# Optimization experiments

Measured on AMD Instinct MI355X. Metric: run time of the kernel, lower is better.

The kernel has to match this reference:

```python
import jax, jax.numpy as jnp
import numpy as np

B, N, M, C = 4, 2048, 576, 512
H, KVH, D = 8, 2, 64          # heads, kv heads, head_dim
E, TOPK, F = 8, 2, 2048       # experts, top-k, expert hidden (4*C)
EPS = 1e-6
NEG = -1e9


def setup_inputs() -> dict:
    key = jax.random.key(0)
    ks = iter(jax.random.split(key, 40))
    w = lambda shape, s=0.02: jax.random.normal(next(ks), shape, jnp.float32) * s
    d = {
        'x': jax.random.normal(next(ks), (B, N, C), jnp.float32),
        'vision_features': jax.random.normal(next(ks), (B, M, C), jnp.float32),
        'ln1_g': jnp.ones((C,), jnp.float32), 'ln1_b': jnp.zeros((C,), jnp.float32),
        'ln2_g': jnp.ones((C,), jnp.float32), 'ln2_b': jnp.zeros((C,), jnp.float32),
        'ln3_g': jnp.ones((C,), jnp.float32), 'ln3_b': jnp.zeros((C,), jnp.float32),
        # self-attention (GQA): q -> C, k/v -> KVH*D
        'sa_wq': w((C, C)), 'sa_bq': jnp.zeros((C,), jnp.float32),
        'sa_wk': w((C, KVH * D)), 'sa_bk': jnp.zeros((KVH * D,), jnp.float32),
        'sa_wv': w((C, KVH * D)), 'sa_bv': jnp.zeros((KVH * D,), jnp.float32),
        'sa_wo': w((C, C)), 'sa_bo': jnp.zeros((C,), jnp.float32),
        # cross-attention (GQA)
        'ca_wq': w((C, C)), 'ca_bq': jnp.zeros((C,), jnp.float32),
        'ca_wk': w((C, KVH * D)), 'ca_bk': jnp.zeros((KVH * D,), jnp.float32),
        'ca_wv': w((C, KVH * D)), 'ca_bv': jnp.zeros((KVH * D,), jnp.float32),
        'ca_wo': w((C, C)), 'ca_bo': jnp.zeros((C,), jnp.float32),
        # MoE: router + stacked expert MLPs (C -> F -> C, GELU)
        'router_w': w((C, E)), 'router_b': jnp.zeros((E,), jnp.float32),
        'e_w1': w((E, C, F)), 'e_b1': jnp.zeros((E, F), jnp.float32),
        'e_w2': w((E, F, C)), 'e_b2': jnp.zeros((E, C), jnp.float32),
    }
    return d


def _ln(x, g, b):
    mu = jnp.mean(x, -1, keepdims=True)
    var = jnp.mean(jnp.square(x - mu), -1, keepdims=True)
    return (x - mu) * jax.lax.rsqrt(var + EPS) * g + b


def _gqa_attn(xq, ctx, wq, bq, wk, bk, wv, bv, wo, bo, causal):
    b, n, c = xq.shape
    m = ctx.shape[1]
    q = (xq @ wq + bq).reshape(b, n, H, D).transpose(0, 2, 1, 3)      # bhnd
    k = (ctx @ wk + bk).reshape(b, m, KVH, D).transpose(0, 2, 1, 3)   # bgmd
    v = (ctx @ wv + bv).reshape(b, m, KVH, D).transpose(0, 2, 1, 3)
    rep = H // KVH
    k = jnp.repeat(k, rep, axis=1)  # repeat_interleave over head dim
    v = jnp.repeat(v, rep, axis=1)
    scores = jnp.einsum('bhnd,bhmd->bhnm', q, k) * (D ** -0.5)
    if causal:
        mask = jnp.tril(jnp.ones((n, m), bool))
        scores = jnp.where(mask, scores, NEG)
    a = jax.nn.softmax(scores, axis=-1)
    o = jnp.einsum('bhnm,bhmd->bhnd', a, v).transpose(0, 2, 1, 3).reshape(b, n, c)
    return o @ wo + bo


def _moe(x, router_w, router_b, e_w1, e_b1, e_w2, e_b2):
    logits = x @ router_w + router_b                    # [B,N,E]
    probs = jax.nn.softmax(logits, axis=-1)
    topv, topi = jax.lax.top_k(probs, TOPK)             # [B,N,K]
    topv = topv / jnp.sum(topv, -1, keepdims=True)      # renormalize top-k gates
    onehot = jax.nn.one_hot(topi, E, dtype=x.dtype)     # [B,N,K,E]
    gates = jnp.einsum('bnke,bnk->bne', onehot, topv)   # sparse gates, zeros off top-k
    h = jax.nn.gelu(jnp.einsum('bnc,ecf->bnef', x, e_w1) + e_b1)
    eo = jnp.einsum('bnef,efc->bnec', h, e_w2) + e_b2
    out = jnp.einsum('bne,bnec->bnc', gates, eo)
    # load-balance aux loss (Switch-style): E * sum_e f_e * P_e
    dispatch = jnp.sum(onehot, axis=2)                  # [B,N,E] routed mask
    f = jnp.mean(dispatch, axis=(0, 1))
    P = jnp.mean(probs, axis=(0, 1))
    aux = E * jnp.sum(f * P)
    return out, aux


def reference(x, vision_features,
              ln1_g, ln1_b, ln2_g, ln2_b, ln3_g, ln3_b,
              sa_wq, sa_bq, sa_wk, sa_bk, sa_wv, sa_bv, sa_wo, sa_bo,
              ca_wq, ca_bq, ca_wk, ca_bk, ca_wv, ca_bv, ca_wo, ca_bo,
              router_w, router_b, e_w1, e_b1, e_w2, e_b2):
    # pre-norm causal self-attn + residual
    h = _ln(x, ln1_g, ln1_b)
    x = x + _gqa_attn(h, h, sa_wq, sa_bq, sa_wk, sa_bk, sa_wv, sa_bv, sa_wo, sa_bo, True)
    # pre-norm cross-attn + residual
    h = _ln(x, ln2_g, ln2_b)
    x = x + _gqa_attn(h, vision_features, ca_wq, ca_bq, ca_wk, ca_bk, ca_wv, ca_bv, ca_wo, ca_bo, False)
    # pre-norm MoE FFN + residual
    h = _ln(x, ln3_g, ln3_b)
    m, aux = _moe(h, router_w, router_b, e_w1, e_b1, e_w2, e_b2)
    return x + m, aux
```

## Files before the change

### kernel.cpp

```cpp
#include <hip/hip_runtime.h>
#include <cstddef>
#include <cstdint>

#define B_   4
#define N_   2048
#define M_   576
#define C_   512
#define H_   8
#define KVH_ 2
#define D_   64
#define E_   8
#define F_   2048
#define BN_  (B_*N_)
#define BM_  (B_*M_)

typedef __attribute__((ext_vector_type(8))) short bf16x8;
typedef __attribute__((ext_vector_type(4))) float f32x4;

__device__ __forceinline__ unsigned short f2bf(float f) {
    union { float f; unsigned int u; } v; v.f = f;
    unsigned int r = v.u + 0x7FFFu + ((v.u >> 16) & 1u);
    return (unsigned short)(r >> 16);
}

__global__ __launch_bounds__(256) void ln_kernel(const float* __restrict__ x,
    const float* __restrict__ g, const float* __restrict__ b, float* __restrict__ out)
{
    int row = blockIdx.x;
    const float* xr = x + (size_t)row * C_;
    float s = 0.f, ss = 0.f;
    for (int c = threadIdx.x; c < C_; c += 256) { float v = xr[c]; s += v; ss += v * v; }
    __shared__ float S1[256], S2[256];
    S1[threadIdx.x] = s; S2[threadIdx.x] = ss;
    __syncthreads();
    for (int o = 128; o > 0; o >>= 1) {
        if (threadIdx.x < o) { S1[threadIdx.x] += S1[threadIdx.x + o]; S2[threadIdx.x] += S2[threadIdx.x + o]; }
        __syncthreads();
    }
    float mu  = S1[0] * (1.f / C_);
    float var = S2[0] * (1.f / C_) - mu * mu;
    float inv = rsqrtf(var + 1e-6f);
    float* orow = out + (size_t)row * C_;
    for (int c = threadIdx.x; c < C_; c += 256)
        orow[c] = (xr[c] - mu) * inv * g[c] + b[c];
}

__global__ __launch_bounds__(256) void ln_bf(const float* __restrict__ x,
    const float* __restrict__ g, const float* __restrict__ b, unsigned short* __restrict__ out)
{
    int row = blockIdx.x;
    const float* xr = x + (size_t)row * C_;
    float s = 0.f, ss = 0.f;
    for (int c = threadIdx.x; c < C_; c += 256) { float v = xr[c]; s += v; ss += v * v; }
    __shared__ float S1[256], S2[256];
    S1[threadIdx.x] = s; S2[threadIdx.x] = ss;
    __syncthreads();
    for (int o = 128; o > 0; o >>= 1) {
        if (threadIdx.x < o) { S1[threadIdx.x] += S1[threadIdx.x + o]; S2[threadIdx.x] += S2[threadIdx.x + o]; }
        __syncthreads();
    }
    float mu  = S1[0] * (1.f / C_);
    float var = S2[0] * (1.f / C_) - mu * mu;
    float inv = rsqrtf(var + 1e-6f);
    unsigned short* orow = out + (size_t)row * C_;
    for (int c = threadIdx.x; c < C_; c += 256)
        orow[c] = f2bf((xr[c] - mu) * inv * g[c] + b[c]);
}

__global__ __launch_bounds__(256) void cast_bf_kernel(const float* __restrict__ in,
    unsigned short* __restrict__ out)
{
    int i = (blockIdx.x * 256 + threadIdx.x) * 4;
    float4 v = *(const float4*)(in + i);
    ushort4 o;
    o.x = f2bf(v.x); o.y = f2bf(v.y); o.z = f2bf(v.z); o.w = f2bf(v.w);
    *(ushort4*)(out + i) = o;
}

__global__ __launch_bounds__(256) void transpose_cast(const float* __restrict__ Win,
    unsigned short* __restrict__ Wtout, int K, int N)
{
    const float* W = Win + (size_t)blockIdx.z * K * N;
    unsigned short* Wt = Wtout + (size_t)blockIdx.z * K * N;
    __shared__ float T[32][33];
    int tid = threadIdx.x;
    int r = tid >> 3, c4 = (tid & 7) * 4;
    int k0 = blockIdx.y * 32, n0 = blockIdx.x * 32;
    float4 v = *(const float4*)&W[(size_t)(k0 + r) * N + n0 + c4];
    T[r][c4 + 0] = v.x; T[r][c4 + 1] = v.y; T[r][c4 + 2] = v.z; T[r][c4 + 3] = v.w;
    __syncthreads();
    ushort4 o;
    o.x = f2bf(T[c4 + 0][r]); o.y = f2bf(T[c4 + 1][r]);
    o.z = f2bf(T[c4 + 2][r]); o.w = f2bf(T[c4 + 3][r]);
    *(ushort4*)&Wt[(size_t)(n0 + r) * K + k0 + c4] = o;
}

__global__ __launch_bounds__(256) void dense_mfma(
    const unsigned short* __restrict__ Abf,
    const unsigned short* __restrict__ Btbf,
    const float* __restrict__ bias,
    float* __restrict__ outF,
    unsigned short* __restrict__ outBf,
    unsigned short* __restrict__ outBf2,
    int N, int K, int mode, int NkPer)
{
    int row0 = blockIdx.y * 128;
    int col0 = blockIdx.x * 128;

    __shared__ unsigned short As[128 * 40];
    __shared__ unsigned short Bs[128 * 40];

    int tid = threadIdx.x;
    int srow = tid >> 2, seg8 = (tid & 3) * 8;
    size_t abase0 = (size_t)(row0 + srow) * K;
    size_t abase1 = (size_t)(row0 + srow + 64) * K;
    size_t bbase0 = (size_t)(col0 + srow) * K;
    size_t bbase1 = (size_t)(col0 + srow + 64) * K;
    int ldsA0 = srow * 40 + seg8, ldsA1 = (srow + 64) * 40 + seg8;

    int lane = tid & 63;
    int wid = tid >> 6;
    int wm0 = (wid & 1) * 64, wn0 = (wid >> 1) * 64;
    int lm = lane & 15, lq = lane >> 4;

    int aoff[4], boff[4];
#pragma unroll
    for (int i = 0; i < 4; i++) {
        aoff[i] = (wm0 + 16 * i + lm) * 40 + lq * 8;
        boff[i] = (wn0 + 16 * i + lm) * 40 + lq * 8;
    }

    f32x4 acc[4][4];
#pragma unroll
    for (int i = 0; i < 4; i++)
#pragma unroll
        for (int j = 0; j < 4; j++)
            acc[i][j] = (f32x4){0.f, 0.f, 0.f, 0.f};

    for (int k0 = 0; k0 < K; k0 += 32) {
        __syncthreads();
        *(uint4*)&As[ldsA0] = *(const uint4*)&Abf[abase0 + k0 + seg8];
        *(uint4*)&As[ldsA1] = *(const uint4*)&Abf[abase1 + k0 + seg8];
        *(uint4*)&Bs[ldsA0] = *(const uint4*)&Btbf[bbase0 + k0 + seg8];
        *(uint4*)&Bs[ldsA1] = *(const uint4*)&Btbf[bbase1 + k0 + seg8];
        __syncthreads();

        bf16x8 av[4], bv[4];
#pragma unroll
        for (int i = 0; i < 4; i++) av[i] = *(const bf16x8*)&As[aoff[i]];
#pragma unroll
        for (int i = 0; i < 4; i++) bv[i] = *(const bf16x8*)&Bs[boff[i]];
#pragma unroll
        for (int mi = 0; mi < 4; mi++)
#pragma unroll
            for (int ni = 0; ni < 4; ni++)
                acc[mi][ni] = __builtin_amdgcn_mfma_f32_16x16x32_bf16(av[mi], bv[ni], acc[mi][ni], 0, 0, 0);
    }

#pragma unroll
    for (int mi = 0; mi < 4; mi++) {
#pragma unroll
        for (int ri = 0; ri < 4; ri++) {
            int gr = row0 + wm0 + 16 * mi + lq * 4 + ri;
            if (mode == 3) {
#pragma unroll
                for (int ni = 0; ni < 4; ni++) {
                    int gc = col0 + wn0 + 16 * ni + lm;
                    float v = acc[mi][ni][ri] + bias[gc];
                    if (gc < 128) {
                        outBf[(size_t)gr * 128 + gc] = f2bf(v);
                    } else {
                        int bb = gr / NkPer;
                        int mm = gr - bb * NkPer;
                        outBf2[((size_t)bb * 128 + (gc - 128)) * NkPer + mm] = f2bf(v);
                    }
                }
            } else if (mode == 2) {
                int bb = gr / NkPer;
                int mm = gr - bb * NkPer;
#pragma unroll
                for (int ni = 0; ni < 4; ni++) {
                    int gc = col0 + wn0 + 16 * ni + lm;
                    outBf[((size_t)bb * (KVH_ * D_) + gc) * NkPer + mm] =
                        f2bf(acc[mi][ni][ri] + bias[gc]);
                }
            } else if (mode == 1) {
                size_t orow = (size_t)gr * N;
#pragma unroll
                for (int ni = 0; ni < 4; ni++) {
                    int gc = col0 + wn0 + 16 * ni + lm;
                    outF[orow + gc] += acc[mi][ni][ri] + bias[gc];
                }
            } else {
                size_t orow = (size_t)gr * N;
#pragma unroll
                for (int ni = 0; ni < 4; ni++) {
                    int gc = col0 + wn0 + 16 * ni + lm;
                    outBf[orow + gc] = f2bf(acc[mi][ni][ri] + bias[gc]);
                }
            }
        }
    }
}

__global__ __launch_bounds__(256) void attn_mfma(
    const unsigned short* __restrict__ Q,
    const unsigned short* __restrict__ K,
    const unsigned short* __restrict__ Vt,
    unsigned short* __restrict__ Obf,
    float* __restrict__ Opart,
    float* __restrict__ Lpart,
    int NkPer, int causal)
{
    __shared__ unsigned short Qs[64 * 72];
    __shared__ unsigned short Ks[64 * 72];
    __shared__ unsigned short Vs[64 * 72];
    unsigned short* Ps = Qs;

    int tid = threadIdx.x;
    int qt = blockIdx.x, bh = blockIdx.y, z = blockIdx.z;
    int b = bh >> 3, h = bh & 7, g = h >> 2;
    int q0 = qt * 64;

#pragma unroll
    for (int i = 0; i < 2; i++) {
        int s = tid + (i << 8);
        int r = s >> 3, c8 = (s & 7) << 3;
        *(uint4*)&Qs[r * 72 + c8] =
            *(const uint4*)&Q[(size_t)(b * N_ + q0 + r) * C_ + h * D_ + c8];
    }
    __syncthreads();

    int lane = tid & 63, wid = tid >> 6;
    int lm = lane & 15, lq = lane >> 4;
    int arow = wid * 16 + lm;

    bf16x8 qf[2];
    qf[0] = *(const bf16x8*)&Qs[arow * 72 + lq * 8];
    qf[1] = *(const bf16x8*)&Qs[arow * 72 + lq * 8 + 32];

    float lsum[4];
    f32x4 of[4];
#pragma unroll
    for (int i = 0; i < 4; i++) { lsum[i] = 0.f; of[i] = (f32x4){0.f,0.f,0.f,0.f}; }

    int nkt = causal ? (qt + 1) : ((NkPer + 63) >> 6);
    int nz = gridDim.z;
    int per = (nkt + nz - 1) / nz;
    int kt0 = z * per;
    int kt1 = min(nkt, kt0 + per);

    for (int kt = kt0; kt < kt1; kt++) {
        int k0 = kt << 6;
        __syncthreads();
#pragma unroll
        for (int i = 0; i < 2; i++) {
            int s = tid + (i << 8);
            int r = s >> 3, c8 = (s & 7) << 3;
            *(uint4*)&Ks[r * 72 + c8] =
                *(const uint4*)&K[(size_t)(b * NkPer + k0 + r) * (KVH_ * D_) + g * D_ + c8];
            *(uint4*)&Vs[r * 72 + c8] =
                *(const uint4*)&Vt[(size_t)(b * (KVH_ * D_) + g * D_ + r) * NkPer + k0 + c8];
        }
        __syncthreads();

        f32x4 sf[4];
#pragma unroll
        for (int i = 0; i < 4; i++) sf[i] = (f32x4){0.f,0.f,0.f,0.f};
#pragma unroll
        for (int ks = 0; ks < 2; ks++) {
#pragma unroll
            for (int ni = 0; ni < 4; ni++) {
                bf16x8 bv = *(const bf16x8*)&Ks[(16 * ni + lm) * 72 + lq * 8 + 32 * ks];
                sf[ni] = __builtin_amdgcn_mfma_f32_16x16x32_bf16(qf[ks], bv, sf[ni], 0, 0, 0);
            }
        }

        bool diag = causal && (k0 + 63 > q0 + wid * 16);
#pragma unroll
        for (int ni = 0; ni < 4; ni++)
#pragma unroll
            for (int ri = 0; ri < 4; ri++) {
                float v = sf[ni][ri] * 0.125f - 8.f;
                if (diag && (k0 + 16 * ni + lm > q0 + wid * 16 + lq * 4 + ri)) v = -1e30f;
                float p = __expf(v);
                sf[ni][ri] = p;
                lsum[ri] += p;
            }

#pragma unroll
        for (int ni = 0; ni < 4; ni++)
#pragma unroll
            for (int ri = 0; ri < 4; ri++)
                Ps[(wid * 16 + lq * 4 + ri) * 72 + 16 * ni + lm] = f2bf(sf[ni][ri]);
        __syncthreads();

        bf16x8 pf0 = *(const bf16x8*)&Ps[arow * 72 + lq * 8];
        bf16x8 pf1 = *(const bf16x8*)&Ps[arow * 72 + lq * 8 + 32];
#pragma unroll
        for (int ni = 0; ni < 4; ni++) {
            bf16x8 vv0 = *(const bf16x8*)&Vs[(16 * ni + lm) * 72 + lq * 8];
            bf16x8 vv1 = *(const bf16x8*)&Vs[(16 * ni + lm) * 72 + lq * 8 + 32];
            of[ni] = __builtin_amdgcn_mfma_f32_16x16x32_bf16(pf0, vv0, of[ni], 0, 0, 0);
            of[ni] = __builtin_amdgcn_mfma_f32_16x16x32_bf16(pf1, vv1, of[ni], 0, 0, 0);
        }
    }

#pragma unroll
    for (int ri = 0; ri < 4; ri++) {
        float s = lsum[ri];
        s += __shfl_xor(s, 1);
        s += __shfl_xor(s, 2);
        s += __shfl_xor(s, 4);
        s += __shfl_xor(s, 8);
        lsum[ri] = s;
    }

    if (nz == 1) {
#pragma unroll
        for (int ri = 0; ri < 4; ri++) {
            float inv = 1.f / lsum[ri];
            int q = q0 + wid * 16 + lq * 4 + ri;
            size_t orow = (size_t)(b * N_ + q) * C_ + h * D_;
#pragma unroll
            for (int ni = 0; ni < 4; ni++)
                Obf[orow + 16 * ni + lm] = f2bf(of[ni][ri] * inv);
        }
    } else {
        size_t zofs = (size_t)z * BN_ * C_;
#pragma unroll
        for (int ri = 0; ri < 4; ri++) {
            int q = q0 + wid * 16 + lq * 4 + ri;
            size_t orow = zofs + (size_t)(b * N_ + q) * C_ + h * D_;
#pragma unroll
            for (int ni = 0; ni < 4; ni++)
                Opart[orow + 16 * ni + lm] = of[ni][ri];
            if (lm == 0)
                Lpart[(size_t)z * (B_ * H_ * N_) + bh * N_ + q] = lsum[ri];
        }
    }
}

__global__ __launch_bounds__(256) void attn_combine(const float* __restrict__ Opart,
    const float* __restrict__ Lpart, unsigned short* __restrict__ Obf)
{
    int flat = (blockIdx.x * 256 + threadIdx.x) * 4;
    int row = flat >> 9, col = flat & 511;
    int b = row >> 11, q = row & (N_ - 1), h = col >> 6;
    int bh = b * 8 + h;
    float l = Lpart[bh * N_ + q] + Lpart[B_ * H_ * N_ + bh * N_ + q];
    float inv = 1.f / l;
    float4 o0 = *(const float4*)&Opart[flat];
    float4 o1 = *(const float4*)&Opart[(size_t)BN_ * C_ + flat];
    ushort4 o;
    o.x = f2bf((o0.x + o1.x) * inv); o.y = f2bf((o0.y + o1.y) * inv);
    o.z = f2bf((o0.z + o1.z) * inv); o.w = f2bf((o0.w + o1.w) * inv);
    *(ushort4*)&Obf[flat] = o;
}

__global__ __launch_bounds__(256) void router_logits(const float* __restrict__ X,
    const float* __restrict__ RW, const float* __restrict__ RB,
    float* __restrict__ gprobs, int* __restrict__ topi, float* __restrict__ gatesv)
{
    int lane = threadIdx.x & 63;
    int t = blockIdx.x * 4 + (threadIdx.x >> 6);
    const float* xr = X + (size_t)t * C_;
    float p[8] = {};
    for (int i = 0; i < 8; i++) {
        int c = i * 64 + lane;
        float xv = xr[c];
#pragma unroll
        for (int e = 0; e < 8; e++) p[e] = fmaf(xv, RW[c * 8 + e], p[e]);
    }
#pragma unroll
    for (int e = 0; e < 8; e++) {
        float v = p[e];
        v += __shfl_xor(v, 32, 64);
        v += __shfl_xor(v, 16, 64);
        v += __shfl_xor(v, 8, 64);
        v += __shfl_xor(v, 4, 64);
        v += __shfl_xor(v, 2, 64);
        v += __shfl_xor(v, 1, 64);
        p[e] = v;
    }
    if (lane == 0) {
        float logits[8], mx = -1e30f;
        for (int e = 0; e < 8; e++) { logits[e] = p[e] + RB[e]; mx = fmaxf(mx, logits[e]); }
        float pr[8], sum = 0.f;
        for (int e = 0; e < 8; e++) { pr[e] = expf(logits[e] - mx); sum += pr[e]; }
        float inv = 1.f / sum;
        for (int e = 0; e < 8; e++) { pr[e] *= inv; gprobs[t * 8 + e] = pr[e]; }
        int i1 = 0;
        for (int e = 1; e < 8; e++) if (pr[e] > pr[i1]) i1 = e;
        int i2 = (i1 == 0) ? 1 : 0;
        for (int e = 0; e < 8; e++) if (e != i1 && pr[e] > pr[i2]) i2 = e;
        float v1 = pr[i1], v2 = pr[i2], sg = 1.f / (v1 + v2);
        topi[t * 2]     = i1;  topi[t * 2 + 1]   = i2;
        gatesv[t * 2]   = v1 * sg;  gatesv[t * 2 + 1] = v2 * sg;
    }
}

__global__ __launch_bounds__(256) void router_reduce(const float* __restrict__ gprobs,
    const int* __restrict__ topi, int* __restrict__ ctrl, float* __restrict__ psum)
{
    __shared__ float fs[256];
    __shared__ int   is_[256];
    int bid = blockIdx.x, tid = threadIdx.x;
    if (bid < 8) {
        float s = 0.f;
        for (int t = tid; t < BN_; t += 256) s += gprobs[t * 8 + bid];
        fs[tid] = s; __syncthreads();
        for (int o = 128; o > 0; o >>= 1) { if (tid < o) fs[tid] += fs[tid + o]; __syncthreads(); }
        if (tid == 0) psum[bid] = fs[0];
    } else {
        int e = bid - 8, c = 0;
        for (int i = tid; i < BN_ * 2; i += 256) c += (topi[i] == e);
        is_[tid] = c; __syncthreads();
        for (int o = 128; o > 0; o >>= 1) { if (tid < o) is_[tid] += is_[tid + o]; __syncthreads(); }
        if (tid == 0) ctrl[e] = is_[0];
    }
}

__global__ void router_offsets(int* __restrict__ ctrl)
{
    if (threadIdx.x == 0 && blockIdx.x == 0) {
        int off = 0;
        for (int e = 0; e < 8; e++) {
            ctrl[16 + e] = off;
            off += (ctrl[e] + 127) & ~127;
        }
        ctrl[24] = off;
    }
}

__global__ __launch_bounds__(256) void router_scatter(const int* __restrict__ topi,
    const float* __restrict__ gatesv, int* __restrict__ rowtok,
    float* __restrict__ rowgate, int* __restrict__ ctrl)
{
    __shared__ int lcnt[8];
    __shared__ int lbase[8];
    int tid = threadIdx.x;
    int t = blockIdx.x * 256 + tid;
    if (tid < 8) lcnt[tid] = 0;
    __syncthreads();
    int e0 = topi[t * 2], e1 = topi[t * 2 + 1];
    int p0 = atomicAdd(&lcnt[e0], 1);
    int p1 = atomicAdd(&lcnt[e1], 1);
    __syncthreads();
    if (tid < 8) lbase[tid] = atomicAdd(&ctrl[8 + tid], lcnt[tid]);
    __syncthreads();
    int s0 = ctrl[16 + e0] + lbase[e0] + p0;
    int s1 = ctrl[16 + e1] + lbase[e1] + p1;
    rowtok[s0] = t; rowgate[s0] = gatesv[t * 2];
    rowtok[s1] = t; rowgate[s1] = gatesv[t * 2 + 1];
}

__global__ __launch_bounds__(256) void moe_mfma(
    const unsigned short* __restrict__ Abf,
    const unsigned short* __restrict__ Btbf,
    const float* __restrict__ biasAll,
    float* __restrict__ outF,
    unsigned short* __restrict__ outBf,
    const int* __restrict__ rowtok,
    const float* __restrict__ rowgate,
    const int* __restrict__ ctrl,
    int N, int K, int mode)
{
    int e = blockIdx.z;
    int cnt = ctrl[e];
    int row0 = blockIdx.y * 128;
    if (row0 >= cnt) return;
    int off = ctrl[16 + e];
    int col0 = blockIdx.x * 128;
    const unsigned short* Bt = Btbf + (size_t)e * N * K;
    const float* bias = biasAll + (size_t)e * N;

    __shared__ unsigned short As[128 * 40];
    __shared__ unsigned short Bs[128 * 40];
    __shared__ int toks[128];

    int tid = threadIdx.x;
    if (mode == 1 && tid < 128) {
        int gl = row0 + tid;
        toks[tid] = rowtok[off + (gl < cnt ? gl : 0)];
    }
    __syncthreads();

    int srow = tid >> 2, seg8 = (tid & 3) * 8;
    size_t abase0, abase1;
    if (mode == 1) {
        abase0 = (size_t)toks[srow] * K;
        abase1 = (size_t)toks[srow + 64] * K;
    } else {
        abase0 = (size_t)(off + row0 + srow) * K;
        abase1 = (size_t)(off + row0 + srow + 64) * K;
    }
    size_t bbase0 = (size_t)(col0 + srow) * K;
    size_t bbase1 = (size_t)(col0 + srow + 64) * K;
    int ldsA0 = srow * 40 + seg8, ldsA1 = (srow + 64) * 40 + seg8;

    int lane = tid & 63;
    int wid = tid >> 6;
    int wm0 = (wid & 1) * 64, wn0 = (wid >> 1) * 64;
    int lm = lane & 15, lq = lane >> 4;

    int aoff[4], boff[4];
#pragma unroll
    for (int i = 0; i < 4; i++) {
        aoff[i] = (wm0 + 16 * i + lm) * 40 + lq * 8;
        boff[i] = (wn0 + 16 * i + lm) * 40 + lq * 8;
    }

    f32x4 acc[4][4];
#pragma unroll
    for (int i = 0; i < 4; i++)
#pragma unroll
        for (int j = 0; j < 4; j++)
            acc[i][j] = (f32x4){0.f, 0.f, 0.f, 0.f};

    for (int k0 = 0; k0 < K; k0 += 32) {
        __syncthreads();
        *(uint4*)&As[ldsA0] = *(const uint4*)&Abf[abase0 + k0 + seg8];
        *(uint4*)&As[ldsA1] = *(const uint4*)&Abf[abase1 + k0 + seg8];
        *(uint4*)&Bs[ldsA0] = *(const uint4*)&Bt[bbase0 + k0 + seg8];
        *(uint4*)&Bs[ldsA1] = *(const uint4*)&Bt[bbase1 + k0 + seg8];
        __syncthreads();

        bf16x8 av[4], bv[4];
#pragma unroll
        for (int i = 0; i < 4; i++) av[i] = *(const bf16x8*)&As[aoff[i]];
#pragma unroll
        for (int i = 0; i < 4; i++) bv[i] = *(const bf16x8*)&Bs[boff[i]];
#pragma unroll
        for (int mi = 0; mi < 4; mi++)
#pragma unroll
            for (int ni = 0; ni < 4; ni++)
                acc[mi][ni] = __builtin_amdgcn_mfma_f32_16x16x32_bf16(av[mi], bv[ni], acc[mi][ni], 0, 0, 0);
    }

#pragma unroll
    for (int mi = 0; mi < 4; mi++) {
#pragma unroll
        for (int ri = 0; ri < 4; ri++) {
            int row_l = wm0 + 16 * mi + lq * 4 + ri;
            int gl = row0 + row_l;
            if (mode == 1) {
                size_t orow = (size_t)(off + gl) * N;
#pragma unroll
                for (int ni = 0; ni < 4; ni++) {
                    int gc = col0 + wn0 + 16 * ni + lm;
                    float hv = 0.f;
                    if (gl < cnt) {
                        float xv = acc[mi][ni][ri] + bias[gc];
                        float x3 = xv * xv * xv;
                        hv = 0.5f * xv * (1.f + tanhf(0.7978845608f * (xv + 0.044715f * x3)));
                    }
                    outBf[orow + gc] = f2bf(hv);
                }
            } else {
                if (gl >= cnt) continue;
                int tok = rowtok[off + gl];
                float gt = rowgate[off + gl];
                size_t orow = (size_t)tok * N;
#pragma unroll
                for (int ni = 0; ni < 4; ni++) {
                    int gc = col0 + wn0 + 16 * ni + lm;
                    atomicAdd(&outF[orow + gc], gt * (acc[mi][ni][ri] + bias[gc]));
                }
            }
        }
    }
}

__global__ void aux_kernel(const int* __restrict__ ctrl, const float* __restrict__ psum,
                           float* __restrict__ outaux)
{
    if (threadIdx.x == 0 && blockIdx.x == 0) {
        float s = 0.f;
        for (int e = 0; e < 8; e++)
            s += ((float)ctrl[e] / (float)BN_) * (psum[e] / (float)BN_);
        outaux[0] = 8.f * s;
    }
}

extern "C" void kernel_launch(void* const* d_in, const int* in_sizes, int n_in,
                              void* d_out, int out_size, void* d_ws, size_t ws_size,
                              hipStream_t stream)
{
    const float* x      = (const float*)d_in[0];
    const float* vis    = (const float*)d_in[1];
    const float* ln1g   = (const float*)d_in[2];
    const float* ln1b   = (const float*)d_in[3];
    const float* ln2g   = (const float*)d_in[4];
    const float* ln2b   = (const float*)d_in[5];
    const float* ln3g   = (const float*)d_in[6];
    const float* ln3b   = (const float*)d_in[7];
    const float* sa_wq  = (const float*)d_in[8];
    const float* sa_bq  = (const float*)d_in[9];
    const float* sa_wk  = (const float*)d_in[10];
    const float* sa_bk  = (const float*)d_in[11];
    const float* sa_wv  = (const float*)d_in[12];
    const float* sa_bv  = (const float*)d_in[13];
    const float* sa_wo  = (const float*)d_in[14];
    const float* sa_bo  = (const float*)d_in[15];
    const float* ca_wq  = (const float*)d_in[16];
    const float* ca_bq  = (const float*)d_in[17];
    const float* ca_wk  = (const float*)d_in[18];
    const float* ca_bk  = (const float*)d_in[19];
    const float* ca_wv  = (const float*)d_in[20];
    const float* ca_bv  = (const float*)d_in[21];
    const float* ca_wo  = (const float*)d_in[22];
    const float* ca_bo  = (const float*)d_in[23];
    const float* rw     = (const float*)d_in[24];
    const float* rb     = (const float*)d_in[25];
    const float* e_w1   = (const float*)d_in[26];
    const float* e_b1   = (const float*)d_in[27];
    const float* e_w2   = (const float*)d_in[28];
    const float* e_b2   = (const float*)d_in[29];

    float* out = (float*)d_out;

    char* ws = (char*)d_ws;
    size_t off = 0;
    auto alloc = [&](size_t bytes) -> void* {
        void* p = ws + off;
        off = (off + bytes + 255) & ~(size_t)255;
        return p;
    };
    float* hbuf    = (float*)alloc((size_t)BN_ * C_ * 4);
    unsigned short* hbz = (unsigned short*)alloc((size_t)BN_ * C_ * 2);
    unsigned short* visbf = (unsigned short*)alloc((size_t)BM_ * C_ * 2);
    char* ureg = (char*)alloc((size_t)17408 * F_ * 2);
    unsigned short* moeH = (unsigned short*)ureg;
    unsigned short* qbf  = (unsigned short*)(ureg);
    unsigned short* obf  = (unsigned short*)(ureg + (size_t)BN_ * C_ * 2);
    unsigned short* kbf  = (unsigned short*)(ureg + (size_t)BN_ * C_ * 4);
    unsigned short* vtbf = (unsigned short*)(ureg + (size_t)BN_ * C_ * 4 + (size_t)BN_ * KVH_ * D_ * 2);
    float* opart = (float*)(ureg + (size_t)BN_ * C_ * 4 + (size_t)BN_ * KVH_ * D_ * 4);
    float* lpart = (float*)(ureg + (size_t)BN_ * C_ * 4 + (size_t)BN_ * KVH_ * D_ * 4
                                 + (size_t)2 * BN_ * C_ * 4);
    unsigned short* sa_wqt = (unsigned short*)alloc((size_t)C_ * C_ * 2);
    unsigned short* sa_wkvt = (unsigned short*)alloc((size_t)C_ * 2 * KVH_ * D_ * 2);
    unsigned short* sa_wot = (unsigned short*)alloc((size_t)C_ * C_ * 2);
    unsigned short* ca_wqt = (unsigned short*)alloc((size_t)C_ * C_ * 2);
    unsigned short* ca_wkvt = (unsigned short*)alloc((size_t)C_ * 2 * KVH_ * D_ * 2);
    unsigned short* ca_wot = (unsigned short*)alloc((size_t)C_ * C_ * 2);
    float* bkv_sa = (float*)alloc(256 * 4);
    float* bkv_ca = (float*)alloc(256 * 4);
    unsigned short* w1t  = (unsigned short*)alloc((size_t)E_ * C_ * F_ * 2);
    unsigned short* w2t  = (unsigned short*)alloc((size_t)E_ * F_ * C_ * 2);
    float* gprobs  = (float*)alloc((size_t)BN_ * 8 * 4);
    int*   topi    = (int*)  alloc((size_t)BN_ * 2 * 4);
    float* gatesv  = (float*)alloc((size_t)BN_ * 2 * 4);
    int*   rowtok  = (int*)  alloc(17408 * 4);
    float* rowgate = (float*)alloc(17408 * 4);
    int*   ctrl    = (int*)  alloc(256);
    float* psum    = (float*)((char*)ctrl + 128);
    (void)ws_size; (void)in_sizes; (void)n_in; (void)out_size;

    hipMemcpyAsync(out, x, (size_t)BN_ * C_ * 4, hipMemcpyDeviceToDevice, stream);

    transpose_cast<<<dim3(16, 16, 1), 256, 0, stream>>>(sa_wq, sa_wqt, C_, C_);
    transpose_cast<<<dim3(4,  16, 1), 256, 0, stream>>>(sa_wk, sa_wkvt, C_, KVH_*D_);
    transpose_cast<<<dim3(4,  16, 1), 256, 0, stream>>>(sa_wv, sa_wkvt + 128 * C_, C_, KVH_*D_);
    transpose_cast<<<dim3(16, 16, 1), 256, 0, stream>>>(sa_wo, sa_wot, C_, C_);
    transpose_cast<<<dim3(16, 16, 1), 256, 0, stream>>>(ca_wq, ca_wqt, C_, C_);
    transpose_cast<<<dim3(4,  16, 1), 256, 0, stream>>>(ca_wk, ca_wkvt, C_, KVH_*D_);
    transpose_cast<<<dim3(4,  16, 1), 256, 0, stream>>>(ca_wv, ca_wkvt + 128 * C_, C_, KVH_*D_);
    transpose_cast<<<dim3(16, 16, 1), 256, 0, stream>>>(ca_wo, ca_wot, C_, C_);
    transpose_cast<<<dim3(F_/32, C_/32, E_), 256, 0, stream>>>(e_w1, w1t, C_, F_);
    transpose_cast<<<dim3(C_/32, F_/32, E_), 256, 0, stream>>>(e_w2, w2t, F_, C_);
    cast_bf_kernel<<<(BM_*C_)/1024, 256, 0, stream>>>(vis, visbf);
    hipMemcpyAsync(bkv_sa,       sa_bk, 128 * 4, hipMemcpyDeviceToDevice, stream);
    hipMemcpyAsync(bkv_sa + 128, sa_bv, 128 * 4, hipMemcpyDeviceToDevice, stream);
    hipMemcpyAsync(bkv_ca,       ca_bk, 128 * 4, hipMemcpyDeviceToDevice, stream);
    hipMemcpyAsync(bkv_ca + 128, ca_bv, 128 * 4, hipMemcpyDeviceToDevice, stream);

    ln_bf<<<BN_, 256, 0, stream>>>(out, ln1g, ln1b, hbz);
    dense_mfma<<<dim3(4, 64), 256, 0, stream>>>(hbz, sa_wqt, sa_bq, nullptr, qbf, nullptr, C_, C_, 0, 0);
    dense_mfma<<<dim3(2, 64), 256, 0, stream>>>(hbz, sa_wkvt, bkv_sa, nullptr, kbf, vtbf, 256, C_, 3, N_);
    attn_mfma<<<dim3(N_/64, B_*H_, 2), 256, 0, stream>>>(qbf, kbf, vtbf, nullptr, opart, lpart, N_, 1);
    attn_combine<<<(BN_*C_)/1024, 256, 0, stream>>>(opart, lpart, obf);
    dense_mfma<<<dim3(4, 64), 256, 0, stream>>>(obf, sa_wot, sa_bo, out, nullptr, nullptr, C_, C_, 1, 0);

    ln_bf<<<BN_, 256, 0, stream>>>(out, ln2g, ln2b, hbz);
    dense_mfma<<<dim3(4, 64), 256, 0, stream>>>(hbz, ca_wqt, ca_bq, nullptr, qbf, nullptr, C_, C_, 0, 0);
    dense_mfma<<<dim3(2, 18), 256, 0, stream>>>(visbf, ca_wkvt, bkv_ca, nullptr, kbf, vtbf, 256, C_, 3, M_);
    attn_mfma<<<dim3(N_/64, B_*H_, 1), 256, 0, stream>>>(qbf, kbf, vtbf, obf, nullptr, nullptr, M_, 0);
    dense_mfma<<<dim3(4, 64), 256, 0, stream>>>(obf, ca_wot, ca_bo, out, nullptr, nullptr, C_, C_, 1, 0);

    ln_kernel<<<BN_, 256, 0, stream>>>(out, ln3g, ln3b, hbuf);
    cast_bf_kernel<<<(BN_*C_)/1024, 256, 0, stream>>>(hbuf, hbz);
    hipMemsetAsync(ctrl, 0, 256, stream);
    router_logits<<<BN_/4, 256, 0, stream>>>(hbuf, rw, rb, gprobs, topi, gatesv);
    router_reduce<<<16, 256, 0, stream>>>(gprobs, topi, ctrl, psum);
    router_offsets<<<1, 1, 0, stream>>>(ctrl);
    router_scatter<<<BN_/256, 256, 0, stream>>>(topi, gatesv, rowtok, rowgate, ctrl);
    moe_mfma<<<dim3(F_/128, BN_/128, E_), 256, 0, stream>>>(
        hbz, w1t, e_b1, nullptr, moeH, rowtok, rowgate, ctrl, F_, C_, 1);
    moe_mfma<<<dim3(C_/128, BN_/128, E_), 256, 0, stream>>>(
        moeH, w2t, e_b2, out, nullptr, rowtok, rowgate, ctrl, C_, F_, 2);
    aux_kernel<<<1, 1, 0, stream>>>(ctrl, psum, out + (size_t)BN_ * C_);
}
```

Baseline: 736.2 us.

## Use direct global-to-LDS loads with swizzle, fuse LN cast, replace MoE atomics with combine

The GEMM kernels now stage tiles with global_load_lds (16-byte direct-to-LDS copies) into an unpadded, XOR-swizzled shared layout instead of register round-trips into padded rows. LN3 writes both fp32 and bf16 outputs in one kernel, removing a separate cast pass. The MoE second GEMM writes per-slot bf16 outputs and a new combine kernel applies gates per token, replacing fp32 atomicAdd scatter. GELU uses an exp-based tanh formulation. The risks are bf16 rounding of expert outputs before gating and correctness of the swizzle mapping.

```diff
diff --git a/kernel.cpp b/kernel.cpp
--- a/kernel.cpp
+++ b/kernel.cpp
@@ -22,9 +22,19 @@
     unsigned int r = v.u + 0x7FFFu + ((v.u >> 16) & 1u);
     return (unsigned short)(r >> 16);
 }
-
-__global__ __launch_bounds__(256) void ln_kernel(const float* __restrict__ x,
-    const float* __restrict__ g, const float* __restrict__ b, float* __restrict__ out)
+__device__ __forceinline__ float bf2f(unsigned short u) {
+    union { unsigned int u; float f; } v; v.u = ((unsigned int)u) << 16;
+    return v.f;
+}
+
+typedef __attribute__((address_space(1))) void glb_void;
+typedef __attribute__((address_space(3))) void lds_void;
+__device__ __forceinline__ void gl2lds16(const unsigned short* g, unsigned short* l) {
+    __builtin_amdgcn_global_load_lds((glb_void*)g, (lds_void*)l, 16, 0, 0);
+}
+
+__global__ __launch_bounds__(256) void ln_bf(const float* __restrict__ x,
+    const float* __restrict__ g, const float* __restrict__ b, unsigned short* __restrict__ out)
 {
     int row = blockIdx.x;
     const float* xr = x + (size_t)row * C_;
@@ -40,13 +50,14 @@
     float mu  = S1[0] * (1.f / C_);
     float var = S2[0] * (1.f / C_) - mu * mu;
     float inv = rsqrtf(var + 1e-6f);
-    float* orow = out + (size_t)row * C_;
+    unsigned short* orow = out + (size_t)row * C_;
     for (int c = threadIdx.x; c < C_; c += 256)
-        orow[c] = (xr[c] - mu) * inv * g[c] + b[c];
-}
-
-__global__ __launch_bounds__(256) void ln_bf(const float* __restrict__ x,
-    const float* __restrict__ g, const float* __restrict__ b, unsigned short* __restrict__ out)
+        orow[c] = f2bf((xr[c] - mu) * inv * g[c] + b[c]);
+}
+
+__global__ __launch_bounds__(256) void ln_dual(const float* __restrict__ x,
+    const float* __restrict__ g, const float* __restrict__ b,
+    float* __restrict__ outF, unsigned short* __restrict__ outBf)
 {
     int row = blockIdx.x;
     const float* xr = x + (size_t)row * C_;
@@ -62,9 +73,11 @@
     float mu  = S1[0] * (1.f / C_);
     float var = S2[0] * (1.f / C_) - mu * mu;
     float inv = rsqrtf(var + 1e-6f);
-    unsigned short* orow = out + (size_t)row * C_;
-    for (int c = threadIdx.x; c < C_; c += 256)
-        orow[c] = f2bf((xr[c] - mu) * inv * g[c] + b[c]);
+    for (int c = threadIdx.x; c < C_; c += 256) {
+        float v = (xr[c] - mu) * inv * g[c] + b[c];
+        outF[(size_t)row * C_ + c] = v;
+        outBf[(size_t)row * C_ + c] = f2bf(v);
+    }
 }
 
 __global__ __launch_bounds__(256) void cast_bf_kernel(const float* __restrict__ in,
@@ -107,27 +120,32 @@
     int row0 = blockIdx.y * 128;
     int col0 = blockIdx.x * 128;
 
-    __shared__ unsigned short As[128 * 40];
-    __shared__ unsigned short Bs[128 * 40];
+    __shared__ unsigned short As[128 * 32];
+    __shared__ unsigned short Bs[128 * 32];
 
     int tid = threadIdx.x;
-    int srow = tid >> 2, seg8 = (tid & 3) * 8;
-    size_t abase0 = (size_t)(row0 + srow) * K;
-    size_t abase1 = (size_t)(row0 + srow + 64) * K;
-    size_t bbase0 = (size_t)(col0 + srow) * K;
-    size_t bbase1 = (size_t)(col0 + srow + 64) * K;
-    int ldsA0 = srow * 40 + seg8, ldsA1 = (srow + 64) * 40 + seg8;
-
-    int lane = tid & 63;
-    int wid = tid >> 6;
+    int lane = tid & 63, wid = tid >> 6;
+    int lrow = lane >> 2;
+    int cswz = (((lane & 3) ^ ((lane >> 3) & 3)) << 3);
+    int ar0 = 16 * (wid * 2) + lrow;
+    int ar1 = ar0 + 16;
+    const unsigned short* gA0 = Abf + (size_t)(row0 + ar0) * K + cswz;
+    const unsigned short* gA1 = Abf + (size_t)(row0 + ar1) * K + cswz;
+    const unsigned short* gB0 = Btbf + (size_t)(col0 + ar0) * K + cswz;
+    const unsigned short* gB1 = Btbf + (size_t)(col0 + ar1) * K + cswz;
+    unsigned short* lA0 = As + (wid * 2) * 512;
+    unsigned short* lA1 = lA0 + 512;
+    unsigned short* lB0 = Bs + (wid * 2) * 512;
+    unsigned short* lB1 = lB0 + 512;
+
     int wm0 = (wid & 1) * 64, wn0 = (wid >> 1) * 64;
     int lm = lane & 15, lq = lane >> 4;
-
+    int swb = (lq ^ ((lm >> 1) & 3)) << 3;
     int aoff[4], boff[4];
 #pragma unroll
     for (int i = 0; i < 4; i++) {
-        aoff[i] = (wm0 + 16 * i + lm) * 40 + lq * 8;
-        boff[i] = (wn0 + 16 * i + lm) * 40 + lq * 8;
+        aoff[i] = (wm0 + 16 * i + lm) * 32 + swb;
+        boff[i] = (wn0 + 16 * i + lm) * 32 + swb;
     }
 
     f32x4 acc[4][4];
@@ -139,10 +157,10 @@
 
     for (int k0 = 0; k0 < K; k0 += 32) {
         __syncthreads();
-        *(uint4*)&As[ldsA0] = *(const uint4*)&Abf[abase0 + k0 + seg8];
-        *(uint4*)&As[ldsA1] = *(const uint4*)&Abf[abase1 + k0 + seg8];
-        *(uint4*)&Bs[ldsA0] = *(const uint4*)&Btbf[bbase0 + k0 + seg8];
-        *(uint4*)&Bs[ldsA1] = *(const uint4*)&Btbf[bbase1 + k0 + seg8];
+        gl2lds16(gA0 + k0, lA0);
+        gl2lds16(gA1 + k0, lA1);
+        gl2lds16(gB0 + k0, lB0);
+        gl2lds16(gB1 + k0, lB1);
         __syncthreads();
 
         bf16x8 av[4], bv[4];
@@ -174,15 +192,6 @@
                         int mm = gr - bb * NkPer;
                         outBf2[((size_t)bb * 128 + (gc - 128)) * NkPer + mm] = f2bf(v);
                     }
-                }
-            } else if (mode == 2) {
-                int bb = gr / NkPer;
-                int mm = gr - bb * NkPer;
-#pragma unroll
-                for (int ni = 0; ni < 4; ni++) {
-                    int gc = col0 + wn0 + 16 * ni + lm;
-                    outBf[((size_t)bb * (KVH_ * D_) + gc) * NkPer + mm] =
-                        f2bf(acc[mi][ni][ri] + bias[gc]);
                 }
             } else if (mode == 1) {
                 size_t orow = (size_t)gr * N;
@@ -435,7 +444,7 @@
 
 __global__ __launch_bounds__(256) void router_scatter(const int* __restrict__ topi,
     const float* __restrict__ gatesv, int* __restrict__ rowtok,
-    float* __restrict__ rowgate, int* __restrict__ ctrl)
+    int* __restrict__ slotidx, int* __restrict__ ctrl)
 {
     __shared__ int lcnt[8];
     __shared__ int lbase[8];
@@ -451,18 +460,18 @@
     __syncthreads();
     int s0 = ctrl[16 + e0] + lbase[e0] + p0;
     int s1 = ctrl[16 + e1] + lbase[e1] + p1;
-    rowtok[s0] = t; rowgate[s0] = gatesv[t * 2];
-    rowtok[s1] = t; rowgate[s1] = gatesv[t * 2 + 1];
+    rowtok[s0] = t;
+    rowtok[s1] = t;
+    slotidx[t * 2]     = s0;
+    slotidx[t * 2 + 1] = s1;
 }
 
 __global__ __launch_bounds__(256) void moe_mfma(
     const unsigned short* __restrict__ Abf,
     const unsigned short* __restrict__ Btbf,
     const float* __restrict__ biasAll,
-    float* __restrict__ outF,
     unsigned short* __restrict__ outBf,
     const int* __restrict__ rowtok,
-    const float* __restrict__ rowgate,
     const int* __restrict__ ctrl,
     int N, int K, int mode)
 {
@@ -475,8 +484,8 @@
     const unsigned short* Bt = Btbf + (size_t)e * N * K;
     const float* bias = biasAll + (size_t)e * N;
 
-    __shared__ unsigned short As[128 * 40];
-    __shared__ unsigned short Bs[128 * 40];
+    __shared__ unsigned short As[128 * 32];
+    __shared__ unsigned short Bs[128 * 32];
     __shared__ int toks[128];
 
     int tid = threadIdx.x;
@@ -486,29 +495,34 @@
     }
     __syncthreads();
 
-    int srow = tid >> 2, seg8 = (tid & 3) * 8;
-    size_t abase0, abase1;
+    int lane = tid & 63, wid = tid >> 6;
+    int lrow = lane >> 2;
+    int cswz = (((lane & 3) ^ ((lane >> 3) & 3)) << 3);
+    int ar0 = 16 * (wid * 2) + lrow;
+    int ar1 = ar0 + 16;
+    const unsigned short *gA0, *gA1;
     if (mode == 1) {
-        abase0 = (size_t)toks[srow] * K;
-        abase1 = (size_t)toks[srow + 64] * K;
+        gA0 = Abf + (size_t)toks[ar0] * K + cswz;
+        gA1 = Abf + (size_t)toks[ar1] * K + cswz;
     } else {
-        abase0 = (size_t)(off + row0 + srow) * K;
-        abase1 = (size_t)(off + row0 + srow + 64) * K;
-    }
-    size_t bbase0 = (size_t)(col0 + srow) * K;
-    size_t bbase1 = (size_t)(col0 + srow + 64) * K;
-    int ldsA0 = srow * 40 + seg8, ldsA1 = (srow + 64) * 40 + seg8;
-
-    int lane = tid & 63;
-    int wid = tid >> 6;
+        gA0 = Abf + (size_t)(off + row0 + ar0) * K + cswz;
+        gA1 = Abf + (size_t)(off + row0 + ar1) * K + cswz;
+    }
+    const unsigned short* gB0 = Bt + (size_t)(col0 + ar0) * K + cswz;
+    const unsigned short* gB1 = Bt + (size_t)(col0 + ar1) * K + cswz;
+    unsigned short* lA0 = As + (wid * 2) * 512;
+    unsigned short* lA1 = lA0 + 512;
+    unsigned short* lB0 = Bs + (wid * 2) * 512;
+    unsigned short* lB1 = lB0 + 512;
+
     int wm0 = (wid & 1) * 64, wn0 = (wid >> 1) * 64;
     int lm = lane & 15, lq = lane >> 4;
-
+    int swb = (lq ^ ((lm >> 1) & 3)) << 3;
     int aoff[4], boff[4];
 #pragma unroll
     for (int i = 0; i < 4; i++) {
-        aoff[i] = (wm0 + 16 * i + lm) * 40 + lq * 8;
-        boff[i] = (wn0 + 16 * i + lm) * 40 + lq * 8;
+        aoff[i] = (wm0 + 16 * i + lm) * 32 + swb;
+        boff[i] = (wn0 + 16 * i + lm) * 32 + swb;
     }
 
     f32x4 acc[4][4];
@@ -520,10 +534,10 @@
 
     for (int k0 = 0; k0 < K; k0 += 32) {
         __syncthreads();
-        *(uint4*)&As[ldsA0] = *(const uint4*)&Abf[abase0 + k0 + seg8];
-        *(uint4*)&As[ldsA1] = *(const uint4*)&Abf[abase1 + k0 + seg8];
-        *(uint4*)&Bs[ldsA0] = *(const uint4*)&Bt[bbase0 + k0 + seg8];
-        *(uint4*)&Bs[ldsA1] = *(const uint4*)&Bt[bbase1 + k0 + seg8];
+        gl2lds16(gA0 + k0, lA0);
+        gl2lds16(gA1 + k0, lA1);
+        gl2lds16(gB0 + k0, lB0);
+        gl2lds16(gB1 + k0, lB1);
         __syncthreads();
 
         bf16x8 av[4], bv[4];
@@ -542,34 +556,47 @@
     for (int mi = 0; mi < 4; mi++) {
 #pragma unroll
         for (int ri = 0; ri < 4; ri++) {
-            int row_l = wm0 + 16 * mi + lq * 4 + ri;
-            int gl = row0 + row_l;
+            int gl = row0 + wm0 + 16 * mi + lq * 4 + ri;
+            size_t orow = (size_t)(off + gl) * N;
             if (mode == 1) {
-                size_t orow = (size_t)(off + gl) * N;
 #pragma unroll
                 for (int ni = 0; ni < 4; ni++) {
                     int gc = col0 + wn0 + 16 * ni + lm;
                     float hv = 0.f;
                     if (gl < cnt) {
                         float xv = acc[mi][ni][ri] + bias[gc];
-                        float x3 = xv * xv * xv;
-                        hv = 0.5f * xv * (1.f + tanhf(0.7978845608f * (xv + 0.044715f * x3)));
+                        float z = 0.7978845608f * xv * fmaf(0.044715f, xv * xv, 1.f);
+                        hv = __fdividef(xv, 1.f + __expf(-2.f * z));
                     }
                     outBf[orow + gc] = f2bf(hv);
                 }
             } else {
-                if (gl >= cnt) continue;
-                int tok = rowtok[off + gl];
-                float gt = rowgate[off + gl];
-                size_t orow = (size_t)tok * N;
 #pragma unroll
                 for (int ni = 0; ni < 4; ni++) {
                     int gc = col0 + wn0 + 16 * ni + lm;
-                    atomicAdd(&outF[orow + gc], gt * (acc[mi][ni][ri] + bias[gc]));
+                    outBf[orow + gc] = f2bf(acc[mi][ni][ri] + bias[gc]);
                 }
             }
         }
     }
+}
+
+__global__ __launch_bounds__(256) void moe_combine(const unsigned short* __restrict__ slots,
+    const int* __restrict__ slotidx, const float* __restrict__ gatesv,
+    float* __restrict__ out)
+{
+    int flat = (blockIdx.x * 256 + threadIdx.x) * 4;
+    int t = flat >> 9, c = flat & 511;
+    int s0 = slotidx[t * 2], s1 = slotidx[t * 2 + 1];
+    float g0 = gatesv[t * 2], g1 = gatesv[t * 2 + 1];
+    ushort4 a = *(const ushort4*)&slots[(size_t)s0 * C_ + c];
+    ushort4 b = *(const ushort4*)&slots[(size_t)s1 * C_ + c];
+    float4 o = *(float4*)&out[flat];
+    o.x += g0 * bf2f(a.x) + g1 * bf2f(b.x);
+    o.y += g0 * bf2f(a.y) + g1 * bf2f(b.y);
+    o.z += g0 * bf2f(a.z) + g1 * bf2f(b.z);
+    o.w += g0 * bf2f(a.w) + g1 * bf2f(b.w);
+    *(float4*)&out[flat] = o;
 }
 
 __global__ void aux_kernel(const int* __restrict__ ctrl, const float* __restrict__ psum,
@@ -630,6 +657,7 @@
     float* hbuf    = (float*)alloc((size_t)BN_ * C_ * 4);
     unsigned short* hbz = (unsigned short*)alloc((size_t)BN_ * C_ * 2);
     unsigned short* visbf = (unsigned short*)alloc((size_t)BM_ * C_ * 2);
+    unsigned short* eoslots = (unsigned short*)hbuf;
     char* ureg = (char*)alloc((size_t)17408 * F_ * 2);
     unsigned short* moeH = (unsigned short*)ureg;
     unsigned short* qbf  = (unsigned short*)(ureg);
@@ -653,7 +681,7 @@
     int*   topi    = (int*)  alloc((size_t)BN_ * 2 * 4);
     float* gatesv  = (float*)alloc((size_t)BN_ * 2 * 4);
     int*   rowtok  = (int*)  alloc(17408 * 4);
-    float* rowgate = (float*)alloc(17408 * 4);
+    int*   slotidx = (int*)  alloc((size_t)BN_ * 2 * 4);
     int*   ctrl    = (int*)  alloc(256);
     float* psum    = (float*)((char*)ctrl + 128);
     (void)ws_size; (void)in_sizes; (void)n_in; (void)out_size;
@@ -689,16 +717,16 @@
     attn_mfma<<<dim3(N_/64, B_*H_, 1), 256, 0, stream>>>(qbf, kbf, vtbf, obf, nullptr, nullptr, M_, 0);
     dense_mfma<<<dim3(4, 64), 256, 0, stream>>>(obf, ca_wot, ca_bo, out, nullptr, nullptr, C_, C_, 1, 0);
 
-    ln_kernel<<<BN_, 256, 0, stream>>>(out, ln3g, ln3b, hbuf);
-    cast_bf_kernel<<<(BN_*C_)/1024, 256, 0, stream>>>(hbuf, hbz);
+    ln_dual<<<BN_, 256, 0, stream>>>(out, ln3g, ln3b, hbuf, hbz);
     hipMemsetAsync(ctrl, 0, 256, stream);
     router_logits<<<BN_/4, 256, 0, stream>>>(hbuf, rw, rb, gprobs, topi, gatesv);
     router_reduce<<<16, 256, 0, stream>>>(gprobs, topi, ctrl, psum);
     router_offsets<<<1, 1, 0, stream>>>(ctrl);
-    router_scatter<<<BN_/256, 256, 0, stream>>>(topi, gatesv, rowtok, rowgate, ctrl);
+    router_scatter<<<BN_/256, 256, 0, stream>>>(topi, gatesv, rowtok, slotidx, ctrl);
     moe_mfma<<<dim3(F_/128, BN_/128, E_), 256, 0, stream>>>(
-        hbz, w1t, e_b1, nullptr, moeH, rowtok, rowgate, ctrl, F_, C_, 1);
+        hbz, w1t, e_b1, moeH, rowtok, ctrl, F_, C_, 1);
     moe_mfma<<<dim3(C_/128, BN_/128, E_), 256, 0, stream>>>(
-        moeH, w2t, e_b2, out, nullptr, rowtok, rowgate, ctrl, C_, F_, 2);
+        moeH, w2t, e_b2, eoslots, rowtok, ctrl, C_, F_, 2);
+    moe_combine<<<(BN_*C_)/1024, 256, 0, stream>>>(eoslots, slotidx, gatesv, out);
     aux_kernel<<<1, 1, 0, stream>>>(ctrl, psum, out + (size_t)BN_ * C_);
 }
```

Result: faster. 698.2 us (-5.2%).
